# Kernel optimization log

Hardware: AMD Instinct MI355X
Metric: run time of the kernel (lower is better)

Reference implementation:

```python
import jax, jax.numpy as jnp
import numpy as np

EPS = 1e-8


def _three_nn_interpolate(coords, ref_coords, features):
    # coords: [B, N, 3], ref_coords: [B, M, 3], features: [B, C, M]
    # squared pairwise distances [B, N, M]
    d2 = (
        jnp.sum(coords * coords, axis=-1, keepdims=True)          # [B, N, 1]
        + jnp.sum(ref_coords * ref_coords, axis=-1)[:, None, :]    # [B, 1, M]
        - 2.0 * jnp.einsum('bnd,bmd->bnm', coords, ref_coords)
    )
    neg_d, idx = jax.lax.top_k(-d2, 3)       # 3 nearest -> idx [B, N, 3]
    dist = -neg_d                             # squared dists of 3-NN
    w = 1.0 / (dist + EPS)
    w = w / jnp.sum(w, axis=-1, keepdims=True)  # [B, N, 3]
    feats_t = jnp.swapaxes(features, 1, 2)    # [B, M, C]
    gathered = jax.vmap(lambda f, i: f[i])(feats_t, idx)  # [B, N, 3, C]
    out = jnp.einsum('bnk,bnkc->bcn', w, gathered)         # [B, C, N]
    return out


def setup_inputs() -> dict:
    key = jax.random.key(0)
    ks = jax.random.split(key, 5)
    B, N, M = 2, 16384, 4096
    return {
        'coords': jax.random.normal(ks[0], (B, N, 3), dtype=jnp.float32),
        'ref_coords': jax.random.normal(ks[1], (B, M, 3), dtype=jnp.float32),
        'ref_features': jax.random.normal(ks[2], (B, 256, M), dtype=jnp.float32),
        'ref_t_embed': jax.random.normal(ks[3], (B, 128, M), dtype=jnp.float32),
        'points_features': jax.random.normal(ks[4], (B, 64, N), dtype=jnp.float32),
    }


def reference(coords, ref_coords, ref_features, ref_t_embed, points_features):
    # PointNetFPModule.forward: interpolate features and t_embed from the
    # coarse ref point set onto the dense point set, then concat skip features.
    features = _three_nn_interpolate(coords, ref_coords, ref_features)  # [B, 256, N]
    t_embed = _three_nn_interpolate(coords, ref_coords, ref_t_embed)    # [B, 128, N]
    features = jnp.concatenate([features, points_features], axis=1)     # [B, 320, N]
    return features, t_embed
```

## Files before the change

kernel.cpp:

```cpp
#include <hip/hip_runtime.h>
#include <cstdint>

#define BB 2
#define NN 16384
#define MM 4096
#define CF 256
#define CT 128
#define CP 64

#define TPB1 512
#define NPB1 64
#define CHUNK 2048

__global__ __launch_bounds__(TPB1, 4) void knn_kernel(
    const float* __restrict__ coords,
    const float* __restrict__ ref_coords,
    int4* __restrict__ wsI,
    float4* __restrict__ wsW)
{
#pragma clang fp contract(off)
    __shared__ float4 refs[CHUNK];

    const int tid = threadIdx.x;
    const int b   = blockIdx.y;
    const int n0  = blockIdx.x * NPB1;

    const int pl = tid >> 3;
    const int s  = tid & 7;
    const int n  = n0 + pl;

    const float* cp = coords + ((size_t)b * NN + n) * 3;
    const float cx = cp[0];
    const float cy = cp[1];
    const float cz = cp[2];
    const float cc = (cx * cx + cy * cy) + cz * cz;

    float d0 = INFINITY, d1 = INFINITY, d2v = INFINITY;
    int   i0 = 0, i1 = 0, i2 = 0;
    float tau = INFINITY;
    float thr = INFINITY;

    const float* rc = ref_coords + (size_t)b * MM * 3;

    for (int ch = 0; ch < MM / CHUNK; ++ch) {
        __syncthreads();
        for (int e = tid; e < CHUNK; e += TPB1) {
            const int j = ch * CHUNK + e;
            const float x = rc[3 * j + 0];
            const float y = rc[3 * j + 1];
            const float z = rc[3 * j + 2];
            refs[e] = make_float4(x + x, y + y, z + z, (x * x + y * y) + z * z);
        }
        __syncthreads();

        const int jbase = ch * CHUNK;
        for (int it0 = 0; it0 < CHUNK / 8; it0 += 32) {
            #pragma unroll 4
            for (int k = 0; k < 32; ++k) {
                const int e = s + ((it0 + k) << 3);
                const float4 r = refs[e];
                const float dot2 = (cx * r.x + cy * r.y) + cz * r.z;
                const float dd   = (cc + r.w) - dot2;
                if (__any(dd < thr)) {
                    const int j = jbase + e;
                    const bool l2 = dd < d2v;
                    const bool l1 = dd < d1;
                    const bool l0 = dd < d0;
                    i2 = l2 ? (l1 ? i1 : j) : i2;
                    i1 = l1 ? (l0 ? i0 : j) : i1;
                    i0 = l0 ? j : i0;
                    const float n2  = __builtin_amdgcn_fmed3f(dd, d1, d2v);
                    const float n1  = __builtin_amdgcn_fmed3f(dd, d0, d1);
                    const float nv0 = fminf(dd, d0);
                    d2v = n2; d1 = n1; d0 = nv0;
                    thr = fminf(d2v, tau);
                }
            }
            float t = d2v;
            t = fminf(t, __shfl_xor(t, 1, 64));
            t = fminf(t, __shfl_xor(t, 2, 64));
            t = fminf(t, __shfl_xor(t, 4, 64));
            tau = t;
            thr = fminf(d2v, tau);
        }
    }

    auto ins = [&](float e, int f) {
        const bool l2 = (e < d2v) || (e == d2v && f < i2);
        const bool l1 = (e < d1)  || (e == d1  && f < i1);
        const bool l0 = (e < d0)  || (e == d0  && f < i0);
        d2v = l2 ? (l1 ? d1 : e) : d2v;  i2 = l2 ? (l1 ? i1 : f) : i2;
        d1  = l1 ? (l0 ? d0 : e) : d1;   i1 = l1 ? (l0 ? i0 : f) : i1;
        d0  = l0 ? e : d0;               i0 = l0 ? f : i0;
    };

    for (int off = 1; off < 8; off <<= 1) {
        const float e0 = __shfl_xor(d0,  off, 64);
        const float e1 = __shfl_xor(d1,  off, 64);
        const float e2 = __shfl_xor(d2v, off, 64);
        const int   f0 = __shfl_xor(i0,  off, 64);
        const int   f1 = __shfl_xor(i1,  off, 64);
        const int   f2 = __shfl_xor(i2,  off, 64);
        ins(e0, f0);
        ins(e1, f1);
        ins(e2, f2);
    }

    if (s == 0) {
        float w0 = 1.0f / (d0  + 1e-8f);
        float w1 = 1.0f / (d1  + 1e-8f);
        float w2 = 1.0f / (d2v + 1e-8f);
        const float sum = (w0 + w1) + w2;
        wsI[(size_t)b * NN + n] = make_int4(i0, i1, i2, 0);
        wsW[(size_t)b * NN + n] = make_float4(w0 / sum, w1 / sum, w2 / sum, 0.0f);
    }
}

#define TPB2 512
#define NIB  (BB * (CF + CT) / 2)
#define NCB  32

__global__ __launch_bounds__(TPB2, 8) void interp_kernel(
    const float* __restrict__ refF,
    const float* __restrict__ refT,
    const float* __restrict__ pf,
    const int4*  __restrict__ wsI,
    const float4* __restrict__ wsW,
    float* __restrict__ out)
{
#pragma clang fp contract(off)
    __shared__ float rowA[MM];
    __shared__ float rowB[MM];
    const int tid  = threadIdx.x;
    const int task = blockIdx.x;
    const size_t outT_base = (size_t)BB * (CF + CP) * NN;

    if (task >= NIB) {
        const int t3 = task - NIB;
        for (int j = 0; j < 4; ++j) {
            const int r  = t3 * 4 + j;
            const int bb = r >> 6;
            const int c  = r & (CP - 1);
            const float4* s4 = (const float4*)(pf + ((size_t)bb * CP + c) * NN);
            float4* d4 = (float4*)(out + ((size_t)bb * (CF + CP) + CF + c) * NN);
            for (int i = tid; i < NN / 4; i += TPB2) d4[i] = s4[i];
        }
        return;
    }

    const int r0 = task * 2;
    const float* src0;
    float* dst0;
    int b;
    if (r0 < BB * CF) {
        b = r0 >> 8;
        const int c = r0 & (CF - 1);
        src0 = refF + ((size_t)b * CF + c) * MM;
        dst0 = out + ((size_t)b * (CF + CP) + c) * NN;
    } else {
        const int r2 = r0 - BB * CF;
        b = r2 >> 7;
        const int c = r2 & (CT - 1);
        src0 = refT + ((size_t)b * CT + c) * MM;
        dst0 = out + outT_base + ((size_t)b * CT + c) * NN;
    }
    const float* src1 = src0 + MM;
    float* dst1 = dst0 + NN;

    for (int i = tid; i < MM / 4; i += TPB2) {
        ((float4*)rowA)[i] = ((const float4*)src0)[i];
        ((float4*)rowB)[i] = ((const float4*)src1)[i];
    }
    __syncthreads();

    const int4*   wi = wsI + (size_t)b * NN;
    const float4* ww = wsW + (size_t)b * NN;

    auto clampi = [](int v) { return v < 0 ? 0 : (v > MM - 1 ? MM - 1 : v); };

    int4   id = wi[tid];
    float4 w  = ww[tid];
    for (int nq = tid; nq < NN; nq += TPB2) {
        const int nq2 = nq + TPB2;
        int4   idn;
        float4 wn;
        if (nq2 < NN) { idn = wi[nq2]; wn = ww[nq2]; }
        const int a0 = clampi(id.x), a1 = clampi(id.y), a2 = clampi(id.z);
        dst0[nq] = (w.x * rowA[a0] + w.y * rowA[a1]) + w.z * rowA[a2];
        dst1[nq] = (w.x * rowB[a0] + w.y * rowB[a1]) + w.z * rowB[a2];
        id = idn; w = wn;
    }
}

extern "C" void kernel_launch(void* const* d_in, const int* in_sizes, int n_in,
                              void* d_out, int out_size, void* d_ws, size_t ws_size,
                              hipStream_t stream) {
    const float* coords     = (const float*)d_in[0];
    const float* ref_coords = (const float*)d_in[1];
    const float* refF       = (const float*)d_in[2];
    const float* refT       = (const float*)d_in[3];
    const float* pf         = (const float*)d_in[4];
    float* out = (float*)d_out;

    int4*   wsI = (int4*)d_ws;
    float4* wsW = (float4*)((char*)d_ws + (size_t)BB * NN * sizeof(int4));

    hipLaunchKernelGGL(knn_kernel, dim3(NN / NPB1, BB), dim3(TPB1), 0, stream,
                       coords, ref_coords, wsI, wsW);
    hipLaunchKernelGGL(interp_kernel, dim3(NIB + NCB), dim3(TPB2), 0, stream,
                       refF, refT, pf, wsI, wsW, out);
}
```

Measured before the change: 160.7 us.

## Bin points by x coordinate and prune kNN search with segment distance bounds

Adds a preprocessing kernel that counting-sorts reference and query points into 256 x-bins, stores the sorted reference coordinates with their original indices, and records x-bounds for 16 segments of 256 references. The kNN kernel then visits segments outward from the query's own x segment and skips any segment whose x-gap already exceeds the current third-best distance for the whole wave. Sorting the queries keeps the lanes of a wave spatially close so they skip the same segments. The extra single-block sort launch (one block per point set per batch) runs mostly serial work, and the 80KB of shared memory per block may limit occupancy.

```diff
diff --git a/kernel.cpp b/kernel.cpp
--- a/kernel.cpp
+++ b/kernel.cpp
@@ -7,29 +7,102 @@
 #define CF 256
 #define CT 128
 #define CP 64
+#define NSEG 16
+#define SEGSZ 256
+
+__global__ __launch_bounds__(512) void sort_kernel(
+    const float* __restrict__ coords,
+    const float* __restrict__ ref_coords,
+    float4* __restrict__ sR,
+    int*    __restrict__ sJ,
+    int*    __restrict__ sQ,
+    float2* __restrict__ segB)
+{
+#pragma clang fp contract(off)
+    __shared__ int hist[256];
+    __shared__ int base_[257];
+    const int tid = threadIdx.x;
+    const int b   = blockIdx.y;
+    const bool doRefs = (blockIdx.x == 0);
+    const int count = doRefs ? MM : NN;
+    const float* src = doRefs ? (ref_coords + (size_t)b * MM * 3)
+                              : (coords     + (size_t)b * NN * 3);
+
+    if (tid < 256) hist[tid] = 0;
+    __syncthreads();
+    for (int e = tid; e < count; e += 512) {
+        const float x = src[3 * e];
+        int bin = (int)((x + 4.5f) * (256.0f / 9.0f));
+        bin = bin < 0 ? 0 : (bin > 255 ? 255 : bin);
+        atomicAdd(&hist[bin], 1);
+    }
+    __syncthreads();
+    if (tid == 0) {
+        int acc = 0;
+        for (int k = 0; k < 256; ++k) { base_[k] = acc; acc += hist[k]; }
+        base_[256] = acc;
+    }
+    __syncthreads();
+    if (tid < 256) hist[tid] = base_[tid];
+    __syncthreads();
+    for (int e = tid; e < count; e += 512) {
+        const float x = src[3 * e];
+        int bin = (int)((x + 4.5f) * (256.0f / 9.0f));
+        bin = bin < 0 ? 0 : (bin > 255 ? 255 : bin);
+        const int pos = atomicAdd(&hist[bin], 1);
+        if (doRefs) {
+            const float y = src[3 * e + 1];
+            const float z = src[3 * e + 2];
+            sR[(size_t)b * MM + pos] = make_float4(x + x, y + y, z + z,
+                                                   (x * x + y * y) + z * z);
+            sJ[(size_t)b * MM + pos] = e;
+        } else {
+            sQ[(size_t)b * NN + pos] = e;
+        }
+    }
+    __syncthreads();
+    if (doRefs && tid == 0) {
+        for (int sg = 0; sg < NSEG; ++sg) {
+            const int plo = sg * SEGSZ, phi = plo + SEGSZ - 1;
+            int blo = 0; while (base_[blo + 1] <= plo) ++blo;
+            int bhi = blo; while (base_[bhi + 1] <= phi) ++bhi;
+            float xlo = (blo == 0)   ? -1e30f : (blo * (9.0f / 256.0f) - 4.5f);
+            float xhi = (bhi == 255) ?  1e30f : ((bhi + 1) * (9.0f / 256.0f) - 4.5f);
+            segB[b * NSEG + sg] = make_float2(xlo, xhi);
+        }
+    }
+}
 
 #define TPB1 512
-#define NPB1 64
-#define CHUNK 2048
 
 __global__ __launch_bounds__(TPB1, 4) void knn_kernel(
     const float* __restrict__ coords,
-    const float* __restrict__ ref_coords,
+    const float4* __restrict__ sR,
+    const int*   __restrict__ sJ,
+    const int*   __restrict__ sQ,
+    const float2* __restrict__ segB,
     int4* __restrict__ wsI,
     float4* __restrict__ wsW)
 {
 #pragma clang fp contract(off)
-    __shared__ float4 refs[CHUNK];
+    __shared__ float4 sref[MM];
+    __shared__ int    sjj[MM];
 
     const int tid = threadIdx.x;
     const int b   = blockIdx.y;
-    const int n0  = blockIdx.x * NPB1;
+
+    for (int e = tid; e < MM; e += TPB1) {
+        sref[e] = sR[(size_t)b * MM + e];
+        sjj[e]  = sJ[(size_t)b * MM + e];
+    }
+    __syncthreads();
 
     const int pl = tid >> 3;
     const int s  = tid & 7;
-    const int n  = n0 + pl;
-
-    const float* cp = coords + ((size_t)b * NN + n) * 3;
+    const int p  = blockIdx.x * 64 + pl;
+    const int qi = sQ[(size_t)b * NN + p];
+
+    const float* cp = coords + ((size_t)b * NN + qi) * 3;
     const float cx = cp[0];
     const float cy = cp[1];
     const float cz = cp[2];
@@ -40,49 +113,49 @@
     float tau = INFINITY;
     float thr = INFINITY;
 
-    const float* rc = ref_coords + (size_t)b * MM * 3;
-
-    for (int ch = 0; ch < MM / CHUNK; ++ch) {
-        __syncthreads();
-        for (int e = tid; e < CHUNK; e += TPB1) {
-            const int j = ch * CHUNK + e;
-            const float x = rc[3 * j + 0];
-            const float y = rc[3 * j + 1];
-            const float z = rc[3 * j + 2];
-            refs[e] = make_float4(x + x, y + y, z + z, (x * x + y * y) + z * z);
-        }
-        __syncthreads();
-
-        const int jbase = ch * CHUNK;
-        for (int it0 = 0; it0 < CHUNK / 8; it0 += 32) {
-            #pragma unroll 4
-            for (int k = 0; k < 32; ++k) {
-                const int e = s + ((it0 + k) << 3);
-                const float4 r = refs[e];
-                const float dot2 = (cx * r.x + cy * r.y) + cz * r.z;
-                const float dd   = (cc + r.w) - dot2;
-                if (__any(dd < thr)) {
-                    const int j = jbase + e;
-                    const bool l2 = dd < d2v;
-                    const bool l1 = dd < d1;
-                    const bool l0 = dd < d0;
-                    i2 = l2 ? (l1 ? i1 : j) : i2;
-                    i1 = l1 ? (l0 ? i0 : j) : i1;
-                    i0 = l0 ? j : i0;
-                    const float n2  = __builtin_amdgcn_fmed3f(dd, d1, d2v);
-                    const float n1  = __builtin_amdgcn_fmed3f(dd, d0, d1);
-                    const float nv0 = fminf(dd, d0);
-                    d2v = n2; d1 = n1; d0 = nv0;
-                    thr = fminf(d2v, tau);
-                }
+    const float xr = __shfl(cx, 32, 64);
+    const float2* sb = segB + b * NSEG;
+    int seg0 = 0;
+    #pragma unroll
+    for (int k = 1; k < NSEG; ++k) seg0 += (sb[k].x <= xr) ? 1 : 0;
+
+    for (int t = 0; t < 2 * NSEG - 1; ++t) {
+        const int o   = (t & 1) ? ((t >> 1) + 1) : -(t >> 1);
+        const int seg = seg0 + o;
+        if (seg < 0 || seg >= NSEG) continue;
+
+        const float2 be = sb[seg];
+        const float dxm = fmaxf(0.0f, fmaxf(be.x - cx, cx - be.y));
+        if (__all(dxm * dxm - 1e-4f > thr)) continue;
+
+        const int ebase = seg * SEGSZ + s;
+        #pragma unroll 4
+        for (int k = 0; k < 32; ++k) {
+            const int e = ebase + (k << 3);
+            const float4 r = sref[e];
+            const float dot2 = (cx * r.x + cy * r.y) + cz * r.z;
+            const float dd   = (cc + r.w) - dot2;
+            if (__any(dd <= thr)) {
+                const int j = sjj[e];
+                const bool l0 = (dd < d0)  || (dd == d0  && j < i0);
+                const bool l1 = (dd < d1)  || (dd == d1  && j < i1);
+                const bool l2 = (dd < d2v) || (dd == d2v && j < i2);
+                i2 = l2 ? (l1 ? i1 : j) : i2;
+                i1 = l1 ? (l0 ? i0 : j) : i1;
+                i0 = l0 ? j : i0;
+                const float n2  = __builtin_amdgcn_fmed3f(dd, d1, d2v);
+                const float n1  = __builtin_amdgcn_fmed3f(dd, d0, d1);
+                const float nv0 = fminf(dd, d0);
+                d2v = n2; d1 = n1; d0 = nv0;
+                thr = fminf(d2v, tau);
             }
-            float t = d2v;
-            t = fminf(t, __shfl_xor(t, 1, 64));
-            t = fminf(t, __shfl_xor(t, 2, 64));
-            t = fminf(t, __shfl_xor(t, 4, 64));
-            tau = t;
-            thr = fminf(d2v, tau);
-        }
+        }
+        float tt = d2v;
+        tt = fminf(tt, __shfl_xor(tt, 1, 64));
+        tt = fminf(tt, __shfl_xor(tt, 2, 64));
+        tt = fminf(tt, __shfl_xor(tt, 4, 64));
+        tau = tt;
+        thr = fminf(d2v, tau);
     }
 
     auto ins = [&](float e, int f) {
@@ -93,7 +166,6 @@
         d1  = l1 ? (l0 ? d0 : e) : d1;   i1 = l1 ? (l0 ? i0 : f) : i1;
         d0  = l0 ? e : d0;               i0 = l0 ? f : i0;
     };
-
     for (int off = 1; off < 8; off <<= 1) {
         const float e0 = __shfl_xor(d0,  off, 64);
         const float e1 = __shfl_xor(d1,  off, 64);
@@ -111,8 +183,8 @@
         float w1 = 1.0f / (d1  + 1e-8f);
         float w2 = 1.0f / (d2v + 1e-8f);
         const float sum = (w0 + w1) + w2;
-        wsI[(size_t)b * NN + n] = make_int4(i0, i1, i2, 0);
-        wsW[(size_t)b * NN + n] = make_float4(w0 / sum, w1 / sum, w2 / sum, 0.0f);
+        wsI[(size_t)b * NN + qi] = make_int4(i0, i1, i2, 0);
+        wsW[(size_t)b * NN + qi] = make_float4(w0 / sum, w1 / sum, w2 / sum, 0.0f);
     }
 }
 
@@ -202,11 +274,18 @@
     const float* pf         = (const float*)d_in[4];
     float* out = (float*)d_out;
 
-    int4*   wsI = (int4*)d_ws;
-    float4* wsW = (float4*)((char*)d_ws + (size_t)BB * NN * sizeof(int4));
-
-    hipLaunchKernelGGL(knn_kernel, dim3(NN / NPB1, BB), dim3(TPB1), 0, stream,
-                       coords, ref_coords, wsI, wsW);
+    char* w = (char*)d_ws;
+    float4* sR   = (float4*)w;                 w += (size_t)BB * MM * sizeof(float4);
+    int*    sJ   = (int*)w;                    w += (size_t)BB * MM * sizeof(int);
+    int*    sQ   = (int*)w;                    w += (size_t)BB * NN * sizeof(int);
+    float2* segB = (float2*)w;                 w += (size_t)BB * NSEG * sizeof(float2);
+    int4*   wsI  = (int4*)w;                   w += (size_t)BB * NN * sizeof(int4);
+    float4* wsW  = (float4*)w;
+
+    hipLaunchKernelGGL(sort_kernel, dim3(2, BB), dim3(512), 0, stream,
+                       coords, ref_coords, sR, sJ, sQ, segB);
+    hipLaunchKernelGGL(knn_kernel, dim3(NN / 64, BB), dim3(TPB1), 0, stream,
+                       coords, sR, sJ, sQ, segB, wsI, wsW);
     hipLaunchKernelGGL(interp_kernel, dim3(NIB + NCB), dim3(TPB2), 0, stream,
                        refF, refT, pf, wsI, wsW, out);
 }
```

New measurement: 268.6 us. 67.1% more time.
